# Kernel tuning notes

Measured on AMD Instinct MI355X. Metric: run time of the kernel, lower is better.

The kernel has to match this reference:

```python
import jax, jax.numpy as jnp
import numpy as np

NUM_USERS = 500000
NUM_ITEMS = 100000
D = 32
NUM_LAYERS = 3
AUDIO_SCALE = 1.0
META_SCALE = 0.5
NUM_ARTISTS = 50000
NUM_ALBUMS = 80000
E_BIP = 1000000


def l2norm(x, eps=1e-12):
    # matches torch F.normalize(p=2): x / max(||x||, eps)
    n = jnp.linalg.norm(x, axis=-1, keepdims=True)
    return x / jnp.maximum(n, eps)


def setup_inputs() -> dict:
    key = jax.random.key(0)
    ks = jax.random.split(key, 9)
    return {
        "user_emb_weight": jax.random.normal(ks[0], (NUM_USERS, D), dtype=jnp.float32),
        "item_audio_emb": jax.random.normal(ks[1], (NUM_ITEMS, D), dtype=jnp.float32),
        "artist_emb_weight": jax.random.normal(ks[2], (NUM_ARTISTS, D), dtype=jnp.float32),
        "album_emb_weight": jax.random.normal(ks[3], (NUM_ALBUMS, D), dtype=jnp.float32),
        "edge_weight": jax.random.uniform(ks[4], (E_BIP,), dtype=jnp.float32),
        "artist_ids": jax.random.randint(ks[5], (NUM_ITEMS,), 0, NUM_ARTISTS),
        "album_ids": jax.random.randint(ks[6], (NUM_ITEMS,), 0, NUM_ALBUMS),
        "edge_src": jax.random.randint(ks[7], (E_BIP,), 0, NUM_USERS),
        "edge_dst": jax.random.randint(ks[8], (E_BIP,), 0, NUM_ITEMS),
    }


def reference(user_emb_weight, item_audio_emb, artist_emb_weight, album_emb_weight,
              edge_weight, artist_ids, album_ids, edge_src, edge_dst):
    N = NUM_USERS + NUM_ITEMS
    # base embeddings
    user = l2norm(user_emb_weight)
    meta = artist_emb_weight[artist_ids] + album_emb_weight[album_ids]
    item = l2norm(item_audio_emb * AUDIO_SCALE + meta * META_SCALE)
    x = jnp.concatenate([user, item], axis=0)  # [N, D]

    # build homogeneous doubled edge list (items offset by NUM_USERS)
    src = jnp.concatenate([edge_src, edge_dst + NUM_USERS])
    dst = jnp.concatenate([edge_dst + NUM_USERS, edge_src])
    w = jnp.concatenate([edge_weight, edge_weight])[:, None]  # [2E, 1]

    acc = x
    for _ in range(NUM_LAYERS):
        # LGConv(normalize=False): out[dst] += w * x[src]
        x = jax.ops.segment_sum(w * x[src], dst, num_segments=N)
        acc = acc + x
    out = l2norm(acc / (NUM_LAYERS + 1))
    user_out = out[:NUM_USERS]
    item_out = out[NUM_USERS:]
    align_loss = jnp.float32(0.0)
    return user_out, item_out, align_loss
```

## Files before the change

kernel.cpp:

```cpp
#include <hip/hip_runtime.h>

constexpr int NUSERS = 500000;
constexpr int NITEMS = 100000;
constexpr int NNODES = NUSERS + NITEMS;
constexpr int EDGES  = 1000000;
constexpr int DIM    = 32;
constexpr long long XSZ = (long long)NNODES * DIM;

constexpr int RSZI = 1000;
constexpr int RI   = NITEMS / RSZI;
constexpr int RSZU = 2000;
constexpr int RU   = NUSERS / RSZU;
constexpr int CAPI = 10800;
constexpr int CAPU = 4600;
constexpr int SLICE = 4096;
constexpr int B1 = (EDGES + SLICE - 1) / SLICE;
constexpr int RBLK4 = (NNODES * 4 + 255) / 256;

using ushort8v = __attribute__((ext_vector_type(8))) unsigned short;
using float4v  = __attribute__((ext_vector_type(4))) float;

__device__ __forceinline__ float bf2f(unsigned short h) {
    return __uint_as_float((unsigned int)h << 16);
}
__device__ __forceinline__ unsigned short f2bf(float f) {
    unsigned int u = __float_as_uint(f);
    u = (u + 0x7FFFu + ((u >> 16) & 1u)) >> 16;
    return (unsigned short)u;
}

__device__ __forceinline__ unsigned int pack_rec(int src, float w) {
    unsigned int wq = (unsigned int)fminf(w * 4096.0f, 4095.0f);
    return ((unsigned int)src << 12) | wq;
}
__device__ __forceinline__ int   rec_src(unsigned int r) { return (int)(r >> 12); }
__device__ __forceinline__ float rec_w(unsigned int r) {
    return ((float)(r & 4095u) + 0.5f) * (1.0f / 4096.0f);
}

__global__ void init_cursor_kernel(int* __restrict__ cursorI, int* __restrict__ cursorU)
{
    int t = threadIdx.x;
    if (t < RI) cursorI[t] = t * CAPI;
    if (t < RU) cursorU[t] = t * CAPU;
}

__global__ void bucket_x0_kernel(
    const int* __restrict__ esrc, const int* __restrict__ edst,
    const float* __restrict__ ew,
    int* __restrict__ cursorI, int* __restrict__ cursorU,
    unsigned int* __restrict__ recBI, unsigned short* __restrict__ locBI,
    unsigned int* __restrict__ recBU, unsigned short* __restrict__ locBU,
    const float* __restrict__ user_w,
    const float* __restrict__ audio,
    const float* __restrict__ artist_w,
    const float* __restrict__ album_w,
    const int*   __restrict__ artist_ids,
    const int*   __restrict__ album_ids,
    unsigned short* __restrict__ x)
{
    __shared__ int histI[RI], histU[RU];
    __shared__ int segI[RI],  segU[RU];
    __shared__ int cntI[RI],  cntU[RU];
    if (blockIdx.x < B1) {
        int tid = threadIdx.x;
        for (int j = tid; j < RI; j += 256) { histI[j] = 0; cntI[j] = 0; }
        for (int j = tid; j < RU; j += 256) { histU[j] = 0; cntU[j] = 0; }
        __syncthreads();

        int base = blockIdx.x * SLICE;
        for (int k = 0; k < SLICE / 256; ++k) {
            int e = base + k * 256 + tid;
            if (e < EDGES) {
                atomicAdd(&histI[edst[e] / RSZI], 1);
                atomicAdd(&histU[esrc[e] / RSZU], 1);
            }
        }
        __syncthreads();
        for (int j = tid; j < RI; j += 256)
            if (histI[j]) segI[j] = atomicAdd(&cursorI[j], histI[j]);
        for (int j = tid; j < RU; j += 256)
            if (histU[j]) segU[j] = atomicAdd(&cursorU[j], histU[j]);
        __syncthreads();
        for (int k = 0; k < SLICE / 256; ++k) {
            int e = base + k * 256 + tid;
            if (e < EDGES) {
                int u = esrc[e], d = edst[e];
                float w = ew[e];
                int rI = d / RSZI;
                int gI = segI[rI] + atomicAdd(&cntI[rI], 1);
                recBI[gI] = pack_rec(u, w);
                locBI[gI] = (unsigned short)(d - rI * RSZI);
                int rU = u / RSZU;
                int gU = segU[rU] + atomicAdd(&cntU[rU], 1);
                recBU[gU] = pack_rec(NUSERS + d, w);
                locBU[gU] = (unsigned short)(u - rU * RSZU);
            }
        }
        return;
    }
    int t   = (blockIdx.x - B1) * 256 + threadIdx.x;
    int row = t >> 2;
    if (row >= NNODES) return;
    int c = (t & 3) << 3;

    float v[8];
    if (row < NUSERS) {
        const float4v* p = (const float4v*)(user_w + (long long)row * DIM + c);
        float4v a = __builtin_nontemporal_load(p);
        float4v b = __builtin_nontemporal_load(p + 1);
        v[0]=a.x; v[1]=a.y; v[2]=a.z; v[3]=a.w;
        v[4]=b.x; v[5]=b.y; v[6]=b.z; v[7]=b.w;
    } else {
        int it = row - NUSERS;
        const float4v* pa = (const float4v*)(audio + (long long)it * DIM + c);
        int ar = artist_ids[it];
        int al = album_ids[it];
        const float* p1 = artist_w + (long long)ar * DIM + c;
        const float* p2 = album_w  + (long long)al * DIM + c;
        float4v a0 = __builtin_nontemporal_load(pa);
        float4v a1 = __builtin_nontemporal_load(pa + 1);
        float4 m0 = *(const float4*)p1,      m1 = *(const float4*)(p1 + 4);
        float4 n0 = *(const float4*)p2,      n1 = *(const float4*)(p2 + 4);
        v[0]=a0.x+0.5f*(m0.x+n0.x); v[1]=a0.y+0.5f*(m0.y+n0.y);
        v[2]=a0.z+0.5f*(m0.z+n0.z); v[3]=a0.w+0.5f*(m0.w+n0.w);
        v[4]=a1.x+0.5f*(m1.x+n1.x); v[5]=a1.y+0.5f*(m1.y+n1.y);
        v[6]=a1.z+0.5f*(m1.z+n1.z); v[7]=a1.w+0.5f*(m1.w+n1.w);
    }

    float ss = 0.f;
    #pragma unroll
    for (int j = 0; j < 8; ++j) ss += v[j] * v[j];
    ss += __shfl_xor(ss, 1);
    ss += __shfl_xor(ss, 2);
    float s = 1.0f / fmaxf(sqrtf(ss), 1e-12f);

    ushort8v hv;
    #pragma unroll
    for (int j = 0; j < 8; ++j) hv[j] = f2bf(v[j] * s);
    *(ushort8v*)(x + (long long)row * DIM + c) = hv;
}

__global__ void rbase_kernel(const int* __restrict__ cursorI,
                             const int* __restrict__ cursorU,
                             int* __restrict__ rbaseI, int* __restrict__ rbaseU,
                             int* __restrict__ offsI, int* __restrict__ offsU)
{
    __shared__ int mI[RI], mU[RU];
    int t = threadIdx.x;
    for (int j = t; j < RI; j += 512) mI[j] = cursorI[j] - j * CAPI;
    for (int j = t; j < RU; j += 512) mU[j] = cursorU[j] - j * CAPU;
    __syncthreads();
    if (t == 0) {
        int s = 0;
        for (int j = 0; j < RI; ++j) { rbaseI[j] = s; s += mI[j]; }
        rbaseI[RI] = s;
        offsI[NITEMS] = s;
    } else if (t == 64) {
        int s = 0;
        for (int j = 0; j < RU; ++j) { rbaseU[j] = s; s += mU[j]; }
        rbaseU[RU] = s;
        offsU[NUSERS] = s;
    }
}

__global__ void finalize_csr_kernel(
    const int* __restrict__ cursorI, const int* __restrict__ cursorU,
    const int* __restrict__ rbaseI, const int* __restrict__ rbaseU,
    const unsigned int* __restrict__ recBI, const unsigned short* __restrict__ locBI,
    const unsigned int* __restrict__ recBU, const unsigned short* __restrict__ locBU,
    int* __restrict__ offsI, int* __restrict__ offsU,
    unsigned int* __restrict__ edI, unsigned int* __restrict__ edU)
{
    __shared__ int deg[RSZU];
    __shared__ int cur[RSZU];
    __shared__ int wsum[512];
    bool item = blockIdx.x < RI;
    int r   = item ? blockIdx.x : blockIdx.x - RI;
    int RSZ = item ? RSZI : RSZU;
    int cap = item ? CAPI : CAPU;
    int bstart = r * cap;
    int m   = (item ? cursorI[r] : cursorU[r]) - bstart;
    int rb  = item ? rbaseI[r] : rbaseU[r];
    const unsigned int*   rec = item ? recBI : recBU;
    const unsigned short* loc = item ? locBI : locBU;
    int* offs = item ? offsI : offsU;
    unsigned int* ed = item ? edI : edU;
    int tid = threadIdx.x;

    for (int j = tid; j < RSZ; j += 512) { deg[j] = 0; cur[j] = 0; }
    __syncthreads();
    for (int k = tid; k < m; k += 512) atomicAdd(&deg[loc[bstart + k]], 1);
    __syncthreads();

    int b4 = tid * 4;
    int v0=0,v1=0,v2=0,v3=0;
    if (b4 + 0 < RSZ) v0 = deg[b4 + 0];
    if (b4 + 1 < RSZ) v1 = deg[b4 + 1];
    if (b4 + 2 < RSZ) v2 = deg[b4 + 2];
    if (b4 + 3 < RSZ) v3 = deg[b4 + 3];
    int lsum = v0 + v1 + v2 + v3;
    wsum[tid] = lsum; __syncthreads();
    for (int ofs = 1; ofs < 512; ofs <<= 1) {
        int add = (tid >= ofs) ? wsum[tid - ofs] : 0;
        __syncthreads();
        wsum[tid] += add;
        __syncthreads();
    }
    int s = wsum[tid] - lsum;
    if (b4 + 0 < RSZ) { deg[b4 + 0] = s; offs[r * RSZ + b4 + 0] = rb + s; s += v0; }
    if (b4 + 1 < RSZ) { deg[b4 + 1] = s; offs[r * RSZ + b4 + 1] = rb + s; s += v1; }
    if (b4 + 2 < RSZ) { deg[b4 + 2] = s; offs[r * RSZ + b4 + 2] = rb + s; s += v2; }
    if (b4 + 3 < RSZ) { deg[b4 + 3] = s; offs[r * RSZ + b4 + 3] = rb + s; s += v3; }
    __syncthreads();

    for (int k = tid; k < m; k += 512) {
        int l = loc[bstart + k];
        int pos = rb + deg[l] + atomicAdd(&cur[l], 1);
        ed[pos] = rec[bstart + k];
    }
}

__device__ __forceinline__ void gather_rows8(
    const unsigned int* __restrict__ ed, int b, int e,
    const unsigned short* __restrict__ xsrc, int c, float* __restrict__ sum)
{
    int k = b;
    for (; k + 3 < e; k += 4) {
        unsigned int r0 = ed[k], r1 = ed[k+1], r2 = ed[k+2], r3 = ed[k+3];
        float w0 = rec_w(r0), w1 = rec_w(r1), w2 = rec_w(r2), w3 = rec_w(r3);
        ushort8v xa = *(const ushort8v*)(xsrc + (long long)rec_src(r0) * DIM + c);
        ushort8v xb = *(const ushort8v*)(xsrc + (long long)rec_src(r1) * DIM + c);
        ushort8v xc = *(const ushort8v*)(xsrc + (long long)rec_src(r2) * DIM + c);
        ushort8v xd = *(const ushort8v*)(xsrc + (long long)rec_src(r3) * DIM + c);
        #pragma unroll
        for (int j = 0; j < 8; ++j)
            sum[j] += (w0 * bf2f(xa[j]) + w1 * bf2f(xb[j]))
                    + (w2 * bf2f(xc[j]) + w3 * bf2f(xd[j]));
    }
    for (; k + 1 < e; k += 2) {
        unsigned int r0 = ed[k], r1 = ed[k+1];
        float w0 = rec_w(r0), w1 = rec_w(r1);
        ushort8v xa = *(const ushort8v*)(xsrc + (long long)rec_src(r0) * DIM + c);
        ushort8v xb = *(const ushort8v*)(xsrc + (long long)rec_src(r1) * DIM + c);
        #pragma unroll
        for (int j = 0; j < 8; ++j)
            sum[j] += w0 * bf2f(xa[j]) + w1 * bf2f(xb[j]);
    }
    if (k < e) {
        unsigned int r0 = ed[k];
        float w0 = rec_w(r0);
        ushort8v xa = *(const ushort8v*)(xsrc + (long long)rec_src(r0) * DIM + c);
        #pragma unroll
        for (int j = 0; j < 8; ++j)
            sum[j] += w0 * bf2f(xa[j]);
    }
}

__global__ void layer_kernel(const int* __restrict__ offsU,
                             const int* __restrict__ offsI,
                             const unsigned int* __restrict__ edU,
                             const unsigned int* __restrict__ edI,
                             const unsigned short* __restrict__ xsrc,
                             unsigned short* __restrict__ xdst)
{
    int t = blockIdx.x * blockDim.x + threadIdx.x;
    int v = t >> 2;
    if (v >= NNODES) return;
    int c = (t & 3) << 3;

    const int* offs; const unsigned int* ed; int idx;
    if (v < NUSERS) { offs = offsU; ed = edU; idx = v; }
    else            { offs = offsI; ed = edI; idx = v - NUSERS; }
    int b = offs[idx], e = offs[idx + 1];

    float sum[8] = {0.f,0.f,0.f,0.f,0.f,0.f,0.f,0.f};
    gather_rows8(ed, b, e, xsrc, c, sum);

    ushort8v hv;
    #pragma unroll
    for (int j = 0; j < 8; ++j) hv[j] = f2bf(sum[j]);
    *(ushort8v*)(xdst + (long long)v * DIM + c) = hv;
}

__global__ void final_kernel(const int* __restrict__ offsU,
                             const int* __restrict__ offsI,
                             const unsigned int* __restrict__ edU,
                             const unsigned int* __restrict__ edI,
                             const unsigned short* __restrict__ x0,
                             const unsigned short* __restrict__ x1,
                             const unsigned short* __restrict__ x2,
                             float* __restrict__ out)
{
    int t = blockIdx.x * blockDim.x + threadIdx.x;
    if (t == 0) out[XSZ] = 0.0f;
    int v = t >> 2;
    if (v >= NNODES) return;
    int c = (t & 3) << 3;

    const int* offs; const unsigned int* ed; int idx;
    if (v < NUSERS) { offs = offsU; ed = edU; idx = v; }
    else            { offs = offsI; ed = edI; idx = v - NUSERS; }
    int b = offs[idx], e = offs[idx + 1];

    float sum[8] = {0.f,0.f,0.f,0.f,0.f,0.f,0.f,0.f};
    gather_rows8(ed, b, e, x2, c, sum);

    long long o = (long long)v * DIM + c;
    ushort8v a0 = __builtin_nontemporal_load((const ushort8v*)(x0 + o));
    ushort8v a1 = __builtin_nontemporal_load((const ushort8v*)(x1 + o));
    ushort8v a2 = *(const ushort8v*)(x2 + o);
    float acc[8];
    float ss = 0.f;
    #pragma unroll
    for (int j = 0; j < 8; ++j) {
        acc[j] = (bf2f(a0[j]) + bf2f(a1[j]) + bf2f(a2[j]) + sum[j]) * 0.25f;
        ss += acc[j] * acc[j];
    }
    ss += __shfl_xor(ss, 1);
    ss += __shfl_xor(ss, 2);
    float s = 1.0f / fmaxf(sqrtf(ss), 1e-12f);

    float4v o0 = { acc[0]*s, acc[1]*s, acc[2]*s, acc[3]*s };
    float4v o1 = { acc[4]*s, acc[5]*s, acc[6]*s, acc[7]*s };
    __builtin_nontemporal_store(o0, (float4v*)(out + o));
    __builtin_nontemporal_store(o1, (float4v*)(out + o + 4));
}

extern "C" void kernel_launch(void* const* d_in, const int* in_sizes, int n_in,
                              void* d_out, int out_size, void* d_ws, size_t ws_size,
                              hipStream_t stream)
{
    const float* user_w     = (const float*)d_in[0];
    const float* audio      = (const float*)d_in[1];
    const float* artist_w   = (const float*)d_in[2];
    const float* album_w    = (const float*)d_in[3];
    const float* ew         = (const float*)d_in[4];
    const int*   artist_ids = (const int*)d_in[5];
    const int*   album_ids  = (const int*)d_in[6];
    const int*   esrc       = (const int*)d_in[7];
    const int*   edst       = (const int*)d_in[8];
    float* out = (float*)d_out;

    unsigned short* x0 = (unsigned short*)d_ws;
    unsigned short* x1 = x0 + XSZ;
    unsigned short* x2 = x1 + XSZ;
    int* offsI = (int*)(x2 + XSZ);
    int* offsU = offsI + (NITEMS + 1);
    int* cursorI = offsU + (NUSERS + 1);
    int* cursorU = cursorI + RI;
    int* rbaseI  = cursorU + RU;
    int* rbaseU  = rbaseI + (RI + 1);
    unsigned int*   recBI = (unsigned int*)(rbaseU + (RU + 1));
    unsigned short* locBI = (unsigned short*)(recBI + (long long)RI * CAPI);
    unsigned int*   recBU = (unsigned int*)(locBI + (long long)RI * CAPI);
    unsigned short* locBU = (unsigned short*)(recBU + (long long)RU * CAPU);
    unsigned int*   edI   = (unsigned int*)(locBU + (long long)RU * CAPU);
    unsigned int*   edU   = edI + EDGES;

    const int THR = 256;

    init_cursor_kernel<<<1, 512, 0, stream>>>(cursorI, cursorU);
    bucket_x0_kernel<<<B1 + RBLK4, THR, 0, stream>>>(
        esrc, edst, ew, cursorI, cursorU, recBI, locBI, recBU, locBU,
        user_w, audio, artist_w, album_w, artist_ids, album_ids, x0);
    rbase_kernel<<<1, 512, 0, stream>>>(
        cursorI, cursorU, rbaseI, rbaseU, offsI, offsU);
    finalize_csr_kernel<<<RI + RU, 512, 0, stream>>>(
        cursorI, cursorU, rbaseI, rbaseU,
        recBI, locBI, recBU, locBU, offsI, offsU, edI, edU);

    layer_kernel<<<RBLK4, THR, 0, stream>>>(offsU, offsI, edU, edI, x0, x1);
    layer_kernel<<<RBLK4, THR, 0, stream>>>(offsU, offsI, edU, edI, x1, x2);
    final_kernel<<<RBLK4, THR, 0, stream>>>(offsU, offsI, edU, edI, x0, x1, x2, out);
}
```

Measured before the change: 225.7 us.

## Replace global atomic cursors with deterministic histogram-scan bucketing

Splits the fused bucket/x0 kernel into separate histogram, per-bucket exclusive scan, and scatter kernels, so each slice-block's offsets into each bucket come from a prefix sum instead of global atomicAdd on shared cursors. x0 normalization becomes its own kernel launched after CSR construction. This removes global atomic contention and makes bucket placement deterministic, but adds kernel launches, a second pass over the edge arrays, and loses the overlap of x0 computation with bucketing.

```diff
diff --git a/kernel.cpp b/kernel.cpp
--- a/kernel.cpp
+++ b/kernel.cpp
@@ -38,19 +38,158 @@
     return ((float)(r & 4095u) + 0.5f) * (1.0f / 4096.0f);
 }
 
-__global__ void init_cursor_kernel(int* __restrict__ cursorI, int* __restrict__ cursorU)
-{
-    int t = threadIdx.x;
-    if (t < RI) cursorI[t] = t * CAPI;
-    if (t < RU) cursorU[t] = t * CAPU;
-}
-
-__global__ void bucket_x0_kernel(
+__global__ void hist_kernel(const int* __restrict__ esrc,
+                            const int* __restrict__ edst,
+                            int* __restrict__ histGI, int* __restrict__ histGU)
+{
+    __shared__ int histI[RI], histU[RU];
+    int tid = threadIdx.x;
+    for (int j = tid; j < RI; j += 256) histI[j] = 0;
+    for (int j = tid; j < RU; j += 256) histU[j] = 0;
+    __syncthreads();
+    int base = blockIdx.x * SLICE;
+    for (int k = 0; k < SLICE / 256; ++k) {
+        int e = base + k * 256 + tid;
+        if (e < EDGES) {
+            atomicAdd(&histI[edst[e] / RSZI], 1);
+            atomicAdd(&histU[esrc[e] / RSZU], 1);
+        }
+    }
+    __syncthreads();
+    for (int j = tid; j < RI; j += 256) histGI[j * B1 + blockIdx.x] = histI[j];
+    for (int j = tid; j < RU; j += 256) histGU[j * B1 + blockIdx.x] = histU[j];
+}
+
+__global__ void base_kernel(int* __restrict__ histGI, int* __restrict__ histGU,
+                            int* __restrict__ mGI, int* __restrict__ mGU)
+{
+    __shared__ int lds[256];
+    bool item = blockIdx.x < RI;
+    int r    = item ? blockIdx.x : blockIdx.x - RI;
+    int* hG  = item ? histGI : histGU;
+    int* mG  = item ? mGI : mGU;
+    int cap  = item ? CAPI : CAPU;
+    int tid  = threadIdx.x;
+    int v = (tid < B1) ? hG[r * B1 + tid] : 0;
+    lds[tid] = v;
+    __syncthreads();
+    for (int ofs = 1; ofs < 256; ofs <<= 1) {
+        int add = (tid >= ofs) ? lds[tid - ofs] : 0;
+        __syncthreads();
+        lds[tid] += add;
+        __syncthreads();
+    }
+    if (tid < B1) hG[r * B1 + tid] = r * cap + (lds[tid] - v);
+    if (tid == 255) mG[r] = lds[255];
+}
+
+__global__ void scatter_kernel(
     const int* __restrict__ esrc, const int* __restrict__ edst,
     const float* __restrict__ ew,
-    int* __restrict__ cursorI, int* __restrict__ cursorU,
+    const int* __restrict__ baseGI, const int* __restrict__ baseGU,
     unsigned int* __restrict__ recBI, unsigned short* __restrict__ locBI,
-    unsigned int* __restrict__ recBU, unsigned short* __restrict__ locBU,
+    unsigned int* __restrict__ recBU, unsigned short* __restrict__ locBU)
+{
+    __shared__ int segI[RI], segU[RU], cntI[RI], cntU[RU];
+    int tid = threadIdx.x;
+    for (int j = tid; j < RI; j += 256) { segI[j] = baseGI[j * B1 + blockIdx.x]; cntI[j] = 0; }
+    for (int j = tid; j < RU; j += 256) { segU[j] = baseGU[j * B1 + blockIdx.x]; cntU[j] = 0; }
+    __syncthreads();
+    int base = blockIdx.x * SLICE;
+    for (int k = 0; k < SLICE / 256; ++k) {
+        int e = base + k * 256 + tid;
+        if (e < EDGES) {
+            int u = esrc[e], d = edst[e];
+            float w = ew[e];
+            int rI = d / RSZI;
+            int gI = segI[rI] + atomicAdd(&cntI[rI], 1);
+            recBI[gI] = pack_rec(u, w);
+            locBI[gI] = (unsigned short)(d - rI * RSZI);
+            int rU = u / RSZU;
+            int gU = segU[rU] + atomicAdd(&cntU[rU], 1);
+            recBU[gU] = pack_rec(NUSERS + d, w);
+            locBU[gU] = (unsigned short)(u - rU * RSZU);
+        }
+    }
+}
+
+__global__ void rbase_kernel(const int* __restrict__ mGI,
+                             const int* __restrict__ mGU,
+                             int* __restrict__ rbaseI, int* __restrict__ rbaseU,
+                             int* __restrict__ offsI, int* __restrict__ offsU)
+{
+    int t = threadIdx.x;
+    if (t == 0) {
+        int s = 0;
+        for (int j = 0; j < RI; ++j) { rbaseI[j] = s; s += mGI[j]; }
+        rbaseI[RI] = s;
+        offsI[NITEMS] = s;
+    } else if (t == 64) {
+        int s = 0;
+        for (int j = 0; j < RU; ++j) { rbaseU[j] = s; s += mGU[j]; }
+        rbaseU[RU] = s;
+        offsU[NUSERS] = s;
+    }
+}
+
+__global__ void finalize_csr_kernel(
+    const int* __restrict__ mGI, const int* __restrict__ mGU,
+    const int* __restrict__ rbaseI, const int* __restrict__ rbaseU,
+    const unsigned int* __restrict__ recBI, const unsigned short* __restrict__ locBI,
+    const unsigned int* __restrict__ recBU, const unsigned short* __restrict__ locBU,
+    int* __restrict__ offsI, int* __restrict__ offsU,
+    unsigned int* __restrict__ edI, unsigned int* __restrict__ edU)
+{
+    __shared__ int deg[RSZU];
+    __shared__ int cur[RSZU];
+    __shared__ int wsum[512];
+    bool item = blockIdx.x < RI;
+    int r   = item ? blockIdx.x : blockIdx.x - RI;
+    int RSZ = item ? RSZI : RSZU;
+    int cap = item ? CAPI : CAPU;
+    int bstart = r * cap;
+    int m   = item ? mGI[r] : mGU[r];
+    int rb  = item ? rbaseI[r] : rbaseU[r];
+    const unsigned int*   rec = item ? recBI : recBU;
+    const unsigned short* loc = item ? locBI : locBU;
+    int* offs = item ? offsI : offsU;
+    unsigned int* ed = item ? edI : edU;
+    int tid = threadIdx.x;
+
+    for (int j = tid; j < RSZ; j += 512) { deg[j] = 0; cur[j] = 0; }
+    __syncthreads();
+    for (int k = tid; k < m; k += 512) atomicAdd(&deg[loc[bstart + k]], 1);
+    __syncthreads();
+
+    int b4 = tid * 4;
+    int v0=0,v1=0,v2=0,v3=0;
+    if (b4 + 0 < RSZ) v0 = deg[b4 + 0];
+    if (b4 + 1 < RSZ) v1 = deg[b4 + 1];
+    if (b4 + 2 < RSZ) v2 = deg[b4 + 2];
+    if (b4 + 3 < RSZ) v3 = deg[b4 + 3];
+    int lsum = v0 + v1 + v2 + v3;
+    wsum[tid] = lsum; __syncthreads();
+    for (int ofs = 1; ofs < 512; ofs <<= 1) {
+        int add = (tid >= ofs) ? wsum[tid - ofs] : 0;
+        __syncthreads();
+        wsum[tid] += add;
+        __syncthreads();
+    }
+    int s = wsum[tid] - lsum;
+    if (b4 + 0 < RSZ) { deg[b4 + 0] = s; offs[r * RSZ + b4 + 0] = rb + s; s += v0; }
+    if (b4 + 1 < RSZ) { deg[b4 + 1] = s; offs[r * RSZ + b4 + 1] = rb + s; s += v1; }
+    if (b4 + 2 < RSZ) { deg[b4 + 2] = s; offs[r * RSZ + b4 + 2] = rb + s; s += v2; }
+    if (b4 + 3 < RSZ) { deg[b4 + 3] = s; offs[r * RSZ + b4 + 3] = rb + s; s += v3; }
+    __syncthreads();
+
+    for (int k = tid; k < m; k += 512) {
+        int l = loc[bstart + k];
+        int pos = rb + deg[l] + atomicAdd(&cur[l], 1);
+        ed[pos] = rec[bstart + k];
+    }
+}
+
+__global__ void x0_kernel(
     const float* __restrict__ user_w,
     const float* __restrict__ audio,
     const float* __restrict__ artist_w,
@@ -59,47 +198,7 @@
     const int*   __restrict__ album_ids,
     unsigned short* __restrict__ x)
 {
-    __shared__ int histI[RI], histU[RU];
-    __shared__ int segI[RI],  segU[RU];
-    __shared__ int cntI[RI],  cntU[RU];
-    if (blockIdx.x < B1) {
-        int tid = threadIdx.x;
-        for (int j = tid; j < RI; j += 256) { histI[j] = 0; cntI[j] = 0; }
-        for (int j = tid; j < RU; j += 256) { histU[j] = 0; cntU[j] = 0; }
-        __syncthreads();
-
-        int base = blockIdx.x * SLICE;
-        for (int k = 0; k < SLICE / 256; ++k) {
-            int e = base + k * 256 + tid;
-            if (e < EDGES) {
-                atomicAdd(&histI[edst[e] / RSZI], 1);
-                atomicAdd(&histU[esrc[e] / RSZU], 1);
-            }
-        }
-        __syncthreads();
-        for (int j = tid; j < RI; j += 256)
-            if (histI[j]) segI[j] = atomicAdd(&cursorI[j], histI[j]);
-        for (int j = tid; j < RU; j += 256)
-            if (histU[j]) segU[j] = atomicAdd(&cursorU[j], histU[j]);
-        __syncthreads();
-        for (int k = 0; k < SLICE / 256; ++k) {
-            int e = base + k * 256 + tid;
-            if (e < EDGES) {
-                int u = esrc[e], d = edst[e];
-                float w = ew[e];
-                int rI = d / RSZI;
-                int gI = segI[rI] + atomicAdd(&cntI[rI], 1);
-                recBI[gI] = pack_rec(u, w);
-                locBI[gI] = (unsigned short)(d - rI * RSZI);
-                int rU = u / RSZU;
-                int gU = segU[rU] + atomicAdd(&cntU[rU], 1);
-                recBU[gU] = pack_rec(NUSERS + d, w);
-                locBU[gU] = (unsigned short)(u - rU * RSZU);
-            }
-        }
-        return;
-    }
-    int t   = (blockIdx.x - B1) * 256 + threadIdx.x;
+    int t   = blockIdx.x * 256 + threadIdx.x;
     int row = t >> 2;
     if (row >= NNODES) return;
     int c = (t & 3) << 3;
@@ -141,86 +240,6 @@
     *(ushort8v*)(x + (long long)row * DIM + c) = hv;
 }
 
-__global__ void rbase_kernel(const int* __restrict__ cursorI,
-                             const int* __restrict__ cursorU,
-                             int* __restrict__ rbaseI, int* __restrict__ rbaseU,
-                             int* __restrict__ offsI, int* __restrict__ offsU)
-{
-    __shared__ int mI[RI], mU[RU];
-    int t = threadIdx.x;
-    for (int j = t; j < RI; j += 512) mI[j] = cursorI[j] - j * CAPI;
-    for (int j = t; j < RU; j += 512) mU[j] = cursorU[j] - j * CAPU;
-    __syncthreads();
-    if (t == 0) {
-        int s = 0;
-        for (int j = 0; j < RI; ++j) { rbaseI[j] = s; s += mI[j]; }
-        rbaseI[RI] = s;
-        offsI[NITEMS] = s;
-    } else if (t == 64) {
-        int s = 0;
-        for (int j = 0; j < RU; ++j) { rbaseU[j] = s; s += mU[j]; }
-        rbaseU[RU] = s;
-        offsU[NUSERS] = s;
-    }
-}
-
-__global__ void finalize_csr_kernel(
-    const int* __restrict__ cursorI, const int* __restrict__ cursorU,
-    const int* __restrict__ rbaseI, const int* __restrict__ rbaseU,
-    const unsigned int* __restrict__ recBI, const unsigned short* __restrict__ locBI,
-    const unsigned int* __restrict__ recBU, const unsigned short* __restrict__ locBU,
-    int* __restrict__ offsI, int* __restrict__ offsU,
-    unsigned int* __restrict__ edI, unsigned int* __restrict__ edU)
-{
-    __shared__ int deg[RSZU];
-    __shared__ int cur[RSZU];
-    __shared__ int wsum[512];
-    bool item = blockIdx.x < RI;
-    int r   = item ? blockIdx.x : blockIdx.x - RI;
-    int RSZ = item ? RSZI : RSZU;
-    int cap = item ? CAPI : CAPU;
-    int bstart = r * cap;
-    int m   = (item ? cursorI[r] : cursorU[r]) - bstart;
-    int rb  = item ? rbaseI[r] : rbaseU[r];
-    const unsigned int*   rec = item ? recBI : recBU;
-    const unsigned short* loc = item ? locBI : locBU;
-    int* offs = item ? offsI : offsU;
-    unsigned int* ed = item ? edI : edU;
-    int tid = threadIdx.x;
-
-    for (int j = tid; j < RSZ; j += 512) { deg[j] = 0; cur[j] = 0; }
-    __syncthreads();
-    for (int k = tid; k < m; k += 512) atomicAdd(&deg[loc[bstart + k]], 1);
-    __syncthreads();
-
-    int b4 = tid * 4;
-    int v0=0,v1=0,v2=0,v3=0;
-    if (b4 + 0 < RSZ) v0 = deg[b4 + 0];
-    if (b4 + 1 < RSZ) v1 = deg[b4 + 1];
-    if (b4 + 2 < RSZ) v2 = deg[b4 + 2];
-    if (b4 + 3 < RSZ) v3 = deg[b4 + 3];
-    int lsum = v0 + v1 + v2 + v3;
-    wsum[tid] = lsum; __syncthreads();
-    for (int ofs = 1; ofs < 512; ofs <<= 1) {
-        int add = (tid >= ofs) ? wsum[tid - ofs] : 0;
-        __syncthreads();
-        wsum[tid] += add;
-        __syncthreads();
-    }
-    int s = wsum[tid] - lsum;
-    if (b4 + 0 < RSZ) { deg[b4 + 0] = s; offs[r * RSZ + b4 + 0] = rb + s; s += v0; }
-    if (b4 + 1 < RSZ) { deg[b4 + 1] = s; offs[r * RSZ + b4 + 1] = rb + s; s += v1; }
-    if (b4 + 2 < RSZ) { deg[b4 + 2] = s; offs[r * RSZ + b4 + 2] = rb + s; s += v2; }
-    if (b4 + 3 < RSZ) { deg[b4 + 3] = s; offs[r * RSZ + b4 + 3] = rb + s; s += v3; }
-    __syncthreads();
-
-    for (int k = tid; k < m; k += 512) {
-        int l = loc[bstart + k];
-        int pos = rb + deg[l] + atomicAdd(&cur[l], 1);
-        ed[pos] = rec[bstart + k];
-    }
-}
-
 __device__ __forceinline__ void gather_rows8(
     const unsigned int* __restrict__ ed, int b, int e,
     const unsigned short* __restrict__ xsrc, int c, float* __restrict__ sum)
@@ -347,10 +366,12 @@
     unsigned short* x2 = x1 + XSZ;
     int* offsI = (int*)(x2 + XSZ);
     int* offsU = offsI + (NITEMS + 1);
-    int* cursorI = offsU + (NUSERS + 1);
-    int* cursorU = cursorI + RI;
-    int* rbaseI  = cursorU + RU;
-    int* rbaseU  = rbaseI + (RI + 1);
+    int* histGI = offsU + (NUSERS + 1);
+    int* histGU = histGI + RI * B1;
+    int* mGI    = histGU + RU * B1;
+    int* mGU    = mGI + RI;
+    int* rbaseI = mGU + RU;
+    int* rbaseU = rbaseI + (RI + 1);
     unsigned int*   recBI = (unsigned int*)(rbaseU + (RU + 1));
     unsigned short* locBI = (unsigned short*)(recBI + (long long)RI * CAPI);
     unsigned int*   recBU = (unsigned int*)(locBI + (long long)RI * CAPI);
@@ -360,15 +381,17 @@
 
     const int THR = 256;
 
-    init_cursor_kernel<<<1, 512, 0, stream>>>(cursorI, cursorU);
-    bucket_x0_kernel<<<B1 + RBLK4, THR, 0, stream>>>(
-        esrc, edst, ew, cursorI, cursorU, recBI, locBI, recBU, locBU,
+    hist_kernel<<<B1, THR, 0, stream>>>(esrc, edst, histGI, histGU);
+    base_kernel<<<RI + RU, 256, 0, stream>>>(histGI, histGU, mGI, mGU);
+    scatter_kernel<<<B1, THR, 0, stream>>>(
+        esrc, edst, ew, histGI, histGU, recBI, locBI, recBU, locBU);
+    rbase_kernel<<<1, 128, 0, stream>>>(mGI, mGU, rbaseI, rbaseU, offsI, offsU);
+    finalize_csr_kernel<<<RI + RU, 512, 0, stream>>>(
+        mGI, mGU, rbaseI, rbaseU,
+        recBI, locBI, recBU, locBU, offsI, offsU, edI, edU);
+
+    x0_kernel<<<RBLK4, THR, 0, stream>>>(
         user_w, audio, artist_w, album_w, artist_ids, album_ids, x0);
-    rbase_kernel<<<1, 512, 0, stream>>>(
-        cursorI, cursorU, rbaseI, rbaseU, offsI, offsU);
-    finalize_csr_kernel<<<RI + RU, 512, 0, stream>>>(
-        cursorI, cursorU, rbaseI, rbaseU,
-        recBI, locBI, recBU, locBU, offsI, offsU, edI, edU);
 
     layer_kernel<<<RBLK4, THR, 0, stream>>>(offsU, offsI, edU, edI, x0, x1);
     layer_kernel<<<RBLK4, THR, 0, stream>>>(offsU, offsI, edU, edI, x1, x2);
```

Result: slower. 233.6 us (+3.5%).
